# Kernel tuning notes

Measured on AMD Instinct MI355X. Metric: run time of the kernel, lower is better.

Reference implementation:

```python
import jax, jax.numpy as jnp
import numpy as np

KERNEL_MUL = 2.0
KERNEL_NUM = 5


def _pairwise_sq_dists(total):
    # ||a-b||^2 = ||a||^2 + ||b||^2 - 2 a.b  (same math as expand-subtract-square-sum)
    sq = jnp.sum(total * total, axis=1)  # [N]
    gram = total @ total.T               # [N, N]
    d2 = sq[:, None] + sq[None, :] - 2.0 * gram
    return jnp.maximum(d2, 0.0)


def setup_inputs() -> dict:
    key = jax.random.key(0)
    k1, k2 = jax.random.split(key)
    source = jax.random.normal(k1, (4096, 256), dtype=jnp.float32)
    target = jax.random.normal(k2, (4096, 256), dtype=jnp.float32)
    return {"source": source, "target": target}


def reference(source, target):
    bs = source.shape[0]
    n_samples = source.shape[0] + target.shape[0]
    total = jnp.concatenate([source, target], axis=0)  # [N, D]
    l2 = _pairwise_sq_dists(total)                      # [N, N]
    # bandwidth computed from detached distances (torch .data)
    bandwidth = jax.lax.stop_gradient(jnp.sum(l2)) / (n_samples ** 2 - n_samples)
    bandwidth = bandwidth / (KERNEL_MUL ** (KERNEL_NUM // 2))
    kernels = jnp.zeros_like(l2)
    for i in range(KERNEL_NUM):
        kernels = kernels + jnp.exp(-l2 / (bandwidth * (KERNEL_MUL ** i)))
    xx = jnp.mean(kernels[:bs, :bs])
    yy = jnp.mean(kernels[bs:, bs:])
    xy = jnp.mean(kernels[:bs, bs:])
    yx = jnp.mean(kernels[bs:, :bs])
    return xx + yy - xy - yx
```

## Files before the change

### kernel.cpp

```cpp
#include <hip/hip_runtime.h>
#include <stdint.h>
#include <stddef.h>


#define N_TOT 8192
#define D_DIM 256
#define BS    4096
#define NB    64
#define NTILE 2080
#define NBLK  512

typedef float  f32x4  __attribute__((ext_vector_type(4)));
typedef short  bf16x8 __attribute__((ext_vector_type(8)));

typedef __attribute__((address_space(1))) const unsigned int gas_u32;
typedef __attribute__((address_space(3))) unsigned int       lds_u32;

__device__ __forceinline__ unsigned short f2bf(float f) {
  unsigned u = __float_as_uint(f);
  u += 0x7fffu + ((u >> 16) & 1u);
  return (unsigned short)(u >> 16);
}
__device__ __forceinline__ float bf2f(unsigned short s) {
  return __uint_as_float(((unsigned)s) << 16);
}

__global__ void prep_kernel(const float* __restrict__ src, const float* __restrict__ tgt,
                            unsigned short* __restrict__ Xbt, float* __restrict__ sq,
                            float* __restrict__ csp) {
  int tid  = threadIdx.x;
  int w    = tid >> 6, lane = tid & 63;
  int blk  = blockIdx.x;
  float4 cacc = {0.f, 0.f, 0.f, 0.f};

  #pragma unroll
  for (int r = 0; r < 4; ++r) {
    int row = blk * 32 + w * 4 + r;
    const float* rowp = (row < BS) ? (src + (size_t)row * D_DIM)
                                   : (tgt + (size_t)(row - BS) * D_DIM);
    float4 v = reinterpret_cast<const float4*>(rowp)[lane];
    cacc.x += v.x; cacc.y += v.y; cacc.z += v.z; cacc.w += v.w;
    ushort4 b;
    b.x = f2bf(v.x); b.y = f2bf(v.y); b.z = f2bf(v.z); b.w = f2bf(v.w);
    int k = lane * 4;
    size_t off = ((size_t)(row >> 4)) * 4096 + (size_t)(k >> 3) * 128
               + (size_t)((row & 15) * 8) + (k & 7);
    *reinterpret_cast<ushort4*>(Xbt + off) = b;
    float fx = bf2f(b.x), fy = bf2f(b.y), fz = bf2f(b.z), fw = bf2f(b.w);
    float s = fx * fx + fy * fy + fz * fz + fw * fw;
    #pragma unroll
    for (int o = 32; o; o >>= 1) s += __shfl_down(s, o, 64);
    if (lane == 0) sq[row] = s;
  }

  __shared__ float cs[8][256];
  reinterpret_cast<float4*>(&cs[w][0])[lane] = cacc;
  __syncthreads();
  if (tid < 256) {
    float s = 0.f;
    #pragma unroll
    for (int ww = 0; ww < 8; ++ww) s += cs[ww][tid];
    csp[blk * 256 + tid] = s;
  }
}

__global__ void bw_kernel(const float* __restrict__ sq, const float* __restrict__ csp,
                          float* __restrict__ coef) {
  int t = threadIdx.x, w = t >> 6, lane = t & 63;
  double s1 = 0.0;
  #pragma unroll
  for (int i = 0; i < 32; ++i) s1 += (double)sq[t + i * 256];
  double c = 0.0;
  #pragma unroll 16
  for (int b = 0; b < 256; ++b) c += (double)csp[b * 256 + t];
  double s2 = c * c;
  #pragma unroll
  for (int o = 32; o; o >>= 1) { s1 += __shfl_down(s1, o, 64); s2 += __shfl_down(s2, o, 64); }
  __shared__ double rs[4], rs2[4];
  if (lane == 0) { rs[w] = s1; rs2[w] = s2; }
  __syncthreads();
  if (t == 0) {
    double S1 = rs[0] + rs[1] + rs[2] + rs[3];
    double S2 = rs2[0] + rs2[1] + rs2[2] + rs2[3];
    double S  = 2.0 * (double)N_TOT * S1 - 2.0 * S2;
    double bw = (S / ((double)N_TOT * (double)N_TOT - (double)N_TOT)) / 4.0;
    *coef = (float)(-1.4426950408889634 / (16.0 * bw));
  }
}

__launch_bounds__(256, 2)
__global__ void gram_kernel(const unsigned short* __restrict__ Xbt, const float* __restrict__ sq,
                            const float* __restrict__ coefp, double* __restrict__ partial) {
  __shared__ __align__(16) unsigned char Alds[65536];

  int tid = threadIdx.x;
  int w = tid >> 6, lane = tid & 63;
  const int lo = lane & 15, hi = lane >> 4;
  const int wr = w >> 1, wc = w & 1;

  int orig = (int)blockIdx.x;
  int blk  = (orig & 7) * (NBLK / 8) + (orig >> 3);

  int first, ntl;
  if (blk < 32) { first = blk * 5; ntl = 5; }
  else          { first = 160 + (blk - 32) * 4; ntl = 4; }

  int bi = 0, rem = first;
  while (rem >= NB - bi) { rem -= NB - bi; ++bi; }
  int bj = bi + rem;

  const char* Xb = (const char*)Xbt;
  float coef = *coefp;
  int bi_staged = -1;
  double dsum = 0.0;

  for (int t = 0; t < ntl; ++t) {
    if (bi != bi_staged) {
      __syncthreads();
      const char* srcA = Xb + (size_t)bi * 65536 + w * 16384 + lane * 16;
      unsigned char* dstA = Alds + w * 16384;
      #pragma unroll
      for (int i = 0; i < 16; ++i)
        __builtin_amdgcn_global_load_lds((gas_u32*)(srcA + i * 1024),
                                         (lds_u32*)(dstA + i * 1024), 16, 0, 0);
      __syncthreads();
      bi_staged = bi;
    }

    float factor = ((bi < 32) == (bj < 32)) ? 1.f : -1.f;
    if (bi != bj) factor *= 2.f;

    const char* pB  = Xb + (size_t)(bj * 8 + wc * 4) * 8192 + (hi * 256 + lo * 16);
    const char* pAl = (const char*)Alds + (size_t)(wr * 4) * 8192 + (hi * 256 + lo * 16);

    f32x4 acc[4][4];
    #pragma unroll
    for (int m = 0; m < 4; ++m)
      #pragma unroll
      for (int n = 0; n < 4; ++n) acc[m][n] = (f32x4){0.f, 0.f, 0.f, 0.f};

    bf16x8 b[4][4], a[2][4];
    #pragma unroll
    for (int s = 0; s < 4; ++s)
      #pragma unroll
      for (int n = 0; n < 4; ++n)
        b[s][n] = *(const bf16x8*)(pB + n * 8192 + s * 1024);
    #pragma unroll
    for (int m = 0; m < 4; ++m) a[0][m] = *(const bf16x8*)(pAl + m * 8192);

    #pragma unroll
    for (int kc = 0; kc < 8; ++kc) {
      if (kc + 1 < 8) {
        #pragma unroll
        for (int m = 0; m < 4; ++m)
          a[(kc + 1) & 1][m] = *(const bf16x8*)(pAl + m * 8192 + (kc + 1) * 1024);
      }
      #pragma unroll
      for (int m = 0; m < 4; ++m)
        #pragma unroll
        for (int n = 0; n < 4; ++n)
          acc[m][n] = __builtin_amdgcn_mfma_f32_16x16x32_bf16(a[kc & 1][m], b[kc & 3][n],
                                                              acc[m][n], 0, 0, 0);
      if (kc + 4 < 8) {
        #pragma unroll
        for (int n = 0; n < 4; ++n)
          b[(kc + 4) & 3][n] = *(const bf16x8*)(pB + n * 8192 + (kc + 4) * 1024);
      }
    }

    float sqj[4], sqi[4][4];
    #pragma unroll
    for (int n = 0; n < 4; ++n) sqj[n] = sq[bj * 128 + wc * 64 + n * 16 + lo];
    #pragma unroll
    for (int m = 0; m < 4; ++m)
      #pragma unroll
      for (int r = 0; r < 4; ++r) sqi[m][r] = sq[bi * 128 + wr * 64 + m * 16 + hi * 4 + r];

    float psum = 0.f;
    #pragma unroll
    for (int m = 0; m < 4; ++m) {
      #pragma unroll
      for (int n = 0; n < 4; ++n) {
        #pragma unroll
        for (int r = 0; r < 4; ++r) {
          float g  = acc[m][n][r];
          float d2 = fmaxf(fmaf(-2.f, g, sqi[m][r] + sqj[n]), 0.f);
          float u  = __builtin_amdgcn_exp2f(d2 * coef);
          float u2 = u * u, u4 = u2 * u2, u8 = u4 * u4, u16 = u8 * u8;
          psum += (u + u2) + (u4 + u8) + u16;
        }
      }
    }
    #pragma unroll
    for (int o = 32; o; o >>= 1) psum += __shfl_down(psum, o, 64);
    if (lane == 0) dsum += (double)(psum * factor);

    ++bj;
    if (bj == NB) { ++bi; bj = bi; }
  }

  __shared__ double wred[4];
  if (lane == 0) wred[w] = dsum;
  __syncthreads();
  if (tid == 0)
    partial[blk] = wred[0] + wred[1] + wred[2] + wred[3];
}

__global__ void reduce_kernel(const double* __restrict__ partial, float* __restrict__ out) {
  int t = threadIdx.x, w = t >> 6, lane = t & 63;
  double s = 0.0;
  for (int i = t; i < NBLK; i += 256) s += partial[i];
  #pragma unroll
  for (int o = 32; o; o >>= 1) s += __shfl_down(s, o, 64);
  __shared__ double rs[4];
  if (lane == 0) rs[w] = s;
  __syncthreads();
  if (t == 0)
    out[0] = (float)((rs[0] + rs[1] + rs[2] + rs[3]) / ((double)BS * (double)BS));
}

extern "C" void kernel_launch(void* const* d_in, const int* in_sizes, int n_in,
                              void* d_out, int out_size, void* d_ws, size_t ws_size,
                              hipStream_t stream) {
  const float* src = (const float*)d_in[0];
  const float* tgt = (const float*)d_in[1];
  char* ws = (char*)d_ws;
  float*  coef    = (float*)(ws + 0);
  double* partial = (double*)(ws + 64);
  float*  csp     = (float*)(ws + 16704);
  float*  sq      = (float*)(ws + 278848);
  unsigned short* Xbt = (unsigned short*)(ws + 311616);
  float* out = (float*)d_out;

  prep_kernel<<<256, 512, 0, stream>>>(src, tgt, Xbt, sq, csp);
  bw_kernel<<<1, 256, 0, stream>>>(sq, csp, coef);
  gram_kernel<<<NBLK, 256, 0, stream>>>(Xbt, sq, coef, partial);
  reduce_kernel<<<1, 256, 0, stream>>>(partial, out);
}
```

Measured before the change: 49.93 us.

## Load A fragments directly from global and widen bandwidth reduction kernel

The gram kernel no longer stages the A row-block into LDS with global_load_lds and barriers. Each wave now reads its A fragments straight from global memory (relying on L2/L1 caching), which removes the LDS footprint and the block-wide syncs but increases global/cache traffic. Separately, the single-block bandwidth reduction kernel is launched with 1024 threads, splitting the column-sum loop into four segments combined through shared memory, to shorten its serial latency. The B prefetch register index is also rewritten to an equivalent slot.

```diff
diff --git a/kernel.cpp b/kernel.cpp
--- a/kernel.cpp
+++ b/kernel.cpp
@@ -12,9 +12,6 @@
 
 typedef float  f32x4  __attribute__((ext_vector_type(4)));
 typedef short  bf16x8 __attribute__((ext_vector_type(8)));
-
-typedef __attribute__((address_space(1))) const unsigned int gas_u32;
-typedef __attribute__((address_space(3))) unsigned int       lds_u32;
 
 __device__ __forceinline__ unsigned short f2bf(float f) {
   unsigned u = __float_as_uint(f);
@@ -67,20 +64,38 @@
 __global__ void bw_kernel(const float* __restrict__ sq, const float* __restrict__ csp,
                           float* __restrict__ coef) {
   int t = threadIdx.x, w = t >> 6, lane = t & 63;
-  double s1 = 0.0;
-  #pragma unroll
-  for (int i = 0; i < 32; ++i) s1 += (double)sq[t + i * 256];
+  int col = t & 255, seg = t >> 8;
+
   double c = 0.0;
   #pragma unroll 16
-  for (int b = 0; b < 256; ++b) c += (double)csp[b * 256 + t];
-  double s2 = c * c;
-  #pragma unroll
-  for (int o = 32; o; o >>= 1) { s1 += __shfl_down(s1, o, 64); s2 += __shfl_down(s2, o, 64); }
-  __shared__ double rs[4], rs2[4];
-  if (lane == 0) { rs[w] = s1; rs2[w] = s2; }
-  __syncthreads();
+  for (int b2 = 0; b2 < 64; ++b2) c += (double)csp[(size_t)(seg * 64 + b2) * 256 + col];
+  __shared__ double csl[4][256];
+  csl[seg][col] = c;
+
+  double s1 = 0.0;
+  #pragma unroll
+  for (int i = 0; i < 8; ++i) s1 += (double)sq[t + i * 1024];
+  #pragma unroll
+  for (int o = 32; o; o >>= 1) s1 += __shfl_down(s1, o, 64);
+  __shared__ double rs[16];
+  if (lane == 0) rs[w] = s1;
+  __syncthreads();
+
+  double S2p = 0.0;
+  if (t < 256) {
+    double cc = csl[0][t] + csl[1][t] + csl[2][t] + csl[3][t];
+    S2p = cc * cc;
+  }
+  #pragma unroll
+  for (int o = 32; o; o >>= 1) S2p += __shfl_down(S2p, o, 64);
+  __shared__ double rs2[4];
+  if (t < 256 && lane == 0) rs2[w] = S2p;
+  __syncthreads();
+
   if (t == 0) {
-    double S1 = rs[0] + rs[1] + rs[2] + rs[3];
+    double S1 = 0.0;
+    #pragma unroll
+    for (int i = 0; i < 16; ++i) S1 += rs[i];
     double S2 = rs2[0] + rs2[1] + rs2[2] + rs2[3];
     double S  = 2.0 * (double)N_TOT * S1 - 2.0 * S2;
     double bw = (S / ((double)N_TOT * (double)N_TOT - (double)N_TOT)) / 4.0;
@@ -91,12 +106,11 @@
 __launch_bounds__(256, 2)
 __global__ void gram_kernel(const unsigned short* __restrict__ Xbt, const float* __restrict__ sq,
                             const float* __restrict__ coefp, double* __restrict__ partial) {
-  __shared__ __align__(16) unsigned char Alds[65536];
-
   int tid = threadIdx.x;
   int w = tid >> 6, lane = tid & 63;
   const int lo = lane & 15, hi = lane >> 4;
   const int wr = w >> 1, wc = w & 1;
+  const int fragoff = hi * 256 + lo * 16;
 
   int orig = (int)blockIdx.x;
   int blk  = (orig & 7) * (NBLK / 8) + (orig >> 3);
@@ -111,27 +125,14 @@
 
   const char* Xb = (const char*)Xbt;
   float coef = *coefp;
-  int bi_staged = -1;
   double dsum = 0.0;
 
   for (int t = 0; t < ntl; ++t) {
-    if (bi != bi_staged) {
-      __syncthreads();
-      const char* srcA = Xb + (size_t)bi * 65536 + w * 16384 + lane * 16;
-      unsigned char* dstA = Alds + w * 16384;
-      #pragma unroll
-      for (int i = 0; i < 16; ++i)
-        __builtin_amdgcn_global_load_lds((gas_u32*)(srcA + i * 1024),
-                                         (lds_u32*)(dstA + i * 1024), 16, 0, 0);
-      __syncthreads();
-      bi_staged = bi;
-    }
-
     float factor = ((bi < 32) == (bj < 32)) ? 1.f : -1.f;
     if (bi != bj) factor *= 2.f;
 
-    const char* pB  = Xb + (size_t)(bj * 8 + wc * 4) * 8192 + (hi * 256 + lo * 16);
-    const char* pAl = (const char*)Alds + (size_t)(wr * 4) * 8192 + (hi * 256 + lo * 16);
+    const char* pA = Xb + (size_t)(bi * 8 + wr * 4) * 8192 + fragoff;
+    const char* pB = Xb + (size_t)(bj * 8 + wc * 4) * 8192 + fragoff;
 
     f32x4 acc[4][4];
     #pragma unroll
@@ -146,14 +147,14 @@
       for (int n = 0; n < 4; ++n)
         b[s][n] = *(const bf16x8*)(pB + n * 8192 + s * 1024);
     #pragma unroll
-    for (int m = 0; m < 4; ++m) a[0][m] = *(const bf16x8*)(pAl + m * 8192);
+    for (int m = 0; m < 4; ++m) a[0][m] = *(const bf16x8*)(pA + m * 8192);
 
     #pragma unroll
     for (int kc = 0; kc < 8; ++kc) {
       if (kc + 1 < 8) {
         #pragma unroll
         for (int m = 0; m < 4; ++m)
-          a[(kc + 1) & 1][m] = *(const bf16x8*)(pAl + m * 8192 + (kc + 1) * 1024);
+          a[(kc + 1) & 1][m] = *(const bf16x8*)(pA + m * 8192 + (kc + 1) * 1024);
       }
       #pragma unroll
       for (int m = 0; m < 4; ++m)
@@ -164,7 +165,7 @@
       if (kc + 4 < 8) {
         #pragma unroll
         for (int n = 0; n < 4; ++n)
-          b[(kc + 4) & 3][n] = *(const bf16x8*)(pB + n * 8192 + (kc + 4) * 1024);
+          b[kc & 3][n] = *(const bf16x8*)(pB + n * 8192 + (kc + 4) * 1024);
       }
     }
 
@@ -233,7 +234,7 @@
   float* out = (float*)d_out;
 
   prep_kernel<<<256, 512, 0, stream>>>(src, tgt, Xbt, sq, csp);
-  bw_kernel<<<1, 256, 0, stream>>>(sq, csp, coef);
+  bw_kernel<<<1, 1024, 0, stream>>>(sq, csp, coef);
   gram_kernel<<<NBLK, 256, 0, stream>>>(Xbt, sq, coef, partial);
   reduce_kernel<<<1, 256, 0, stream>>>(partial, out);
 }
```

Result: slower. 62.29 us (+24.8%).
